# Kernel tuning notes

Hardware: AMD Instinct MI355X
Metric: run time of the kernel (lower is better)

Reference implementation:

```python
import jax, jax.numpy as jnp
import numpy as np

N_NODES = 50000
N_EDGES = 600000
D_IN = 128
D_OUT = 128


def setup_inputs() -> dict:
    key = jax.random.key(0)
    ks = jax.random.split(key, 6)
    gain = float(np.sqrt(2.0))  # relu gain for xavier init
    lim = gain * np.sqrt(6.0 / (D_IN + D_IN))
    pool_w = jax.random.uniform(ks[0], (D_IN, D_IN), jnp.float32, -lim, lim)
    lim2 = gain * np.sqrt(6.0 / (D_IN + D_OUT))
    lin_w = jax.random.uniform(ks[1], (D_OUT, D_IN), jnp.float32, -lim2, lim2)
    return {
        "node_feats": jax.random.normal(ks[2], (N_NODES, D_IN), jnp.float32),
        "src": jax.random.randint(ks[3], (N_EDGES,), 0, N_NODES, jnp.int32),
        "dst": jax.random.randint(ks[4], (N_EDGES,), 0, N_NODES, jnp.int32),
        "e_weight": jax.random.uniform(ks[5], (N_EDGES,), jnp.float32),
        "pool_w": pool_w,
        "pool_b": jnp.zeros((D_IN,), jnp.float32),
        "lin_w": lin_w,
        "lin_b": jnp.zeros((D_OUT,), jnp.float32),
        "bias": jnp.zeros((D_OUT,), jnp.float32),
    }


def reference(node_feats, src, dst, e_weight, pool_w, pool_b, lin_w, lin_b, bias):
    # maxpool aggregator: h_src = relu(pool(x) + pool_bias)   [N, D_IN]
    h_src = jax.nn.relu(node_feats @ pool_w.T + pool_b)
    # u_mul_e message: gather src features, scale by edge weight  [E, D_IN]
    m = h_src[src] * e_weight[:, None]
    # fn.max reduce per destination node; empty mailboxes -> 0
    h_new = jax.ops.segment_max(m, dst, num_segments=N_NODES)
    h_new = jnp.where(jnp.isfinite(h_new), h_new, 0.0)
    # final linear (+its bias) + extra bias parameter
    return h_new @ lin_w.T + lin_b + bias
```

## Files before the change

kernel.cpp:

```cpp
#include <hip/hip_runtime.h>
#include <hip/hip_bf16.h>

#define NN 50000
#define NE 600000
#define DD 128
#define CAP 48

typedef __attribute__((ext_vector_type(8))) short short8_t;
typedef __attribute__((ext_vector_type(4))) short short4_t;
typedef __attribute__((ext_vector_type(4))) float f32x4;

__device__ __forceinline__ short f2bf(float f) {
    union { float f; unsigned u; } v; v.f = f;
    unsigned r = (v.u + 0x7FFFu + ((v.u >> 16) & 1u)) >> 16;
    return (short)r;
}
__device__ __forceinline__ float bflo(unsigned x) { return __uint_as_float(x << 16); }
__device__ __forceinline__ float bfhi(unsigned x) { return __uint_as_float(x & 0xffff0000u); }

__device__ __forceinline__ void gl16(const void* g, void* l) {
    __builtin_amdgcn_global_load_lds(
        (const __attribute__((address_space(1))) unsigned*)g,
        (__attribute__((address_space(3))) unsigned*)l, 16, 0, 0);
}

__global__ __launch_bounds__(512) void gemm1(const float* __restrict__ A,
        const float* __restrict__ Wp, const float* __restrict__ b1,
        unsigned short* __restrict__ hout, const float* __restrict__ Wl,
        unsigned short* __restrict__ wimg, int* __restrict__ counts)
{
    __shared__ short aL[128 * 128];
    __shared__ short wL[128 * 128];
    const int tid = threadIdx.x;
    const int m0 = blockIdx.x * 128;

    {
        int gid = blockIdx.x * 512 + tid;
        if (gid < NN) counts[gid] = 0;
    }
    if (blockIdx.x == 0) {
        #pragma unroll
        for (int i = 0; i < 8; ++i) {
            int idx = (i * 512 + tid) * 4;
            int row = idx >> 7;
            int kk = (idx & 127) ^ ((row & 7) << 3);
            float4 v = *(const float4*)(Wl + row * 128 + kk);
            short4_t s4 = { f2bf(v.x), f2bf(v.y), f2bf(v.z), f2bf(v.w) };
            *(short4_t*)(wimg + idx) = s4;
        }
    }

    #pragma unroll
    for (int i = 0; i < 8; ++i) {
        int flat = i * 2048 + tid * 4;
        int row = flat >> 7, k = flat & 127;
        int gr = m0 + row;
        float4 v = make_float4(0.f, 0.f, 0.f, 0.f);
        if (gr < NN) v = *(const float4*)(A + (size_t)gr * 128 + k);
        short4_t s4 = { f2bf(v.x), f2bf(v.y), f2bf(v.z), f2bf(v.w) };
        *(short4_t*)(aL + ((row * 128 + k) ^ ((row & 7) << 3))) = s4;
    }
    #pragma unroll
    for (int i = 0; i < 8; ++i) {
        int flat = i * 2048 + tid * 4;
        int row = flat >> 7, k = flat & 127;
        float4 v = *(const float4*)(Wp + flat);
        short4_t s4 = { f2bf(v.x), f2bf(v.y), f2bf(v.z), f2bf(v.w) };
        *(short4_t*)(wL + ((row * 128 + k) ^ ((row & 7) << 3))) = s4;
    }
    __syncthreads();

    const int lane = tid & 63, wid = tid >> 6;
    const int l15 = lane & 15, lhi = lane >> 4;
    const int r0 = wid * 16;
    f32x4 acc[8];
    #pragma unroll
    for (int t = 0; t < 8; ++t) acc[t] = f32x4{0.f, 0.f, 0.f, 0.f};

    #pragma unroll
    for (int kk = 0; kk < 4; ++kk) {
        const int k0 = kk * 32 + lhi * 8;
        const int ar = r0 + l15;
        short8_t a = *(short8_t*)(aL + ((ar * 128 + k0) ^ ((ar & 7) << 3)));
        #pragma unroll
        for (int t = 0; t < 8; ++t) {
            const int br = t * 16 + l15;
            short8_t b = *(short8_t*)(wL + ((br * 128 + k0) ^ ((br & 7) << 3)));
            acc[t] = __builtin_amdgcn_mfma_f32_16x16x32_bf16(a, b, acc[t], 0, 0, 0);
        }
    }

    #pragma unroll
    for (int t = 0; t < 8; ++t) {
        const int c = t * 16 + l15;
        float add = b1[c];
        #pragma unroll
        for (int i = 0; i < 4; ++i) {
            int r = m0 + r0 + lhi * 4 + i;
            if (r < NN) {
                float v = fmaxf(acc[t][i] + add, 0.f);
                hout[(size_t)r * 128 + (c ^ ((r & 7) << 3))] = (unsigned short)f2bf(v);
            }
        }
    }
}

__global__ __launch_bounds__(256) void bucket(const int* __restrict__ src,
        const int* __restrict__ dst, const float* __restrict__ ew,
        int* __restrict__ counts, unsigned* __restrict__ edges)
{
    int e = blockIdx.x * 256 + threadIdx.x;
    if (e >= NE) return;
    int d = dst[e];
    int pos = atomicAdd(&counts[d], 1);
    if (pos < CAP)
        edges[(size_t)d * CAP + pos] =
            ((unsigned)src[e] << 16) | (unsigned short)f2bf(ew[e]);
}

template<int NIT>
__device__ __forceinline__ void gat(const unsigned short* __restrict__ hb,
        unsigned p, int deg, int g, int l16, float* m)
{
    #pragma unroll
    for (int it = 0; it < NIT; ++it) {
        const int ia = it * 8 + g, ib = it * 8 + 4 + g;
        unsigned pa = __shfl(p, ia), pb = __shfl(p, ib);
        float wa = (ia < deg) ? __uint_as_float(pa << 16) : 0.f;
        float wb = (ib < deg) ? __uint_as_float(pb << 16) : 0.f;
        unsigned sa = pa >> 16, sb = pb >> 16;
        uint4 ra = *(const uint4*)(hb + (size_t)sa * 128 + ((l16 * 8) ^ ((sa & 7) << 3)));
        uint4 rb = *(const uint4*)(hb + (size_t)sb * 128 + ((l16 * 8) ^ ((sb & 7) << 3)));
        m[0] = fmaxf(m[0], bflo(ra.x) * wa); m[1] = fmaxf(m[1], bfhi(ra.x) * wa);
        m[2] = fmaxf(m[2], bflo(ra.y) * wa); m[3] = fmaxf(m[3], bfhi(ra.y) * wa);
        m[4] = fmaxf(m[4], bflo(ra.z) * wa); m[5] = fmaxf(m[5], bfhi(ra.z) * wa);
        m[6] = fmaxf(m[6], bflo(ra.w) * wa); m[7] = fmaxf(m[7], bfhi(ra.w) * wa);
        m[0] = fmaxf(m[0], bflo(rb.x) * wb); m[1] = fmaxf(m[1], bfhi(rb.x) * wb);
        m[2] = fmaxf(m[2], bflo(rb.y) * wb); m[3] = fmaxf(m[3], bfhi(rb.y) * wb);
        m[4] = fmaxf(m[4], bflo(rb.z) * wb); m[5] = fmaxf(m[5], bfhi(rb.z) * wb);
        m[6] = fmaxf(m[6], bflo(rb.w) * wb); m[7] = fmaxf(m[7], bfhi(rb.w) * wb);
    }
}

__global__ __launch_bounds__(256) void node_max(const unsigned short* __restrict__ hb,
        const int* __restrict__ counts, const unsigned* __restrict__ edges,
        unsigned short* __restrict__ hnew)
{
    int node = blockIdx.x * 4 + (threadIdx.x >> 6);
    if (node >= NN) return;
    const int lane = threadIdx.x & 63;
    const int g = lane >> 4, l16 = lane & 15;
    const int deg = min(counts[node], CAP);
    const unsigned* ep = edges + (size_t)node * CAP;
    unsigned p = (lane < deg) ? ep[lane] : 0u;

    float m[8];
    #pragma unroll
    for (int i = 0; i < 8; ++i) m[i] = 0.f;

    if (deg <= 16)      gat<2>(hb, p, deg, g, l16, m);
    else if (deg <= 32) gat<4>(hb, p, deg, g, l16, m);
    else                gat<6>(hb, p, deg, g, l16, m);

    #pragma unroll
    for (int i = 0; i < 8; ++i) {
        m[i] = fmaxf(m[i], __shfl_xor(m[i], 16));
        m[i] = fmaxf(m[i], __shfl_xor(m[i], 32));
    }

    if (g == 0) {
        uint4 o;
        o.x = ((unsigned)(unsigned short)f2bf(m[1]) << 16) | (unsigned short)f2bf(m[0]);
        o.y = ((unsigned)(unsigned short)f2bf(m[3]) << 16) | (unsigned short)f2bf(m[2]);
        o.z = ((unsigned)(unsigned short)f2bf(m[5]) << 16) | (unsigned short)f2bf(m[4]);
        o.w = ((unsigned)(unsigned short)f2bf(m[7]) << 16) | (unsigned short)f2bf(m[6]);
        *(uint4*)(hnew + (size_t)node * 128 + ((l16 * 8) ^ ((node & 7) << 3))) = o;
    }
}

__global__ __launch_bounds__(512) void gemm2(const unsigned short* __restrict__ Aimg,
        const unsigned short* __restrict__ wimg, const float* __restrict__ b1,
        const float* __restrict__ b2, float* __restrict__ out)
{
    __shared__ short aL[128 * 128];
    __shared__ short wL[128 * 128];
    const int tid = threadIdx.x;
    const int lane = tid & 63, wid = tid >> 6;
    const int m0 = blockIdx.x * 128;

    #pragma unroll
    for (int i = 0; i < 4; ++i) {
        const int soff = i * 4096 + wid * 512;
        gl16(Aimg + (size_t)m0 * 128 + soff + lane * 8, aL + soff);
        gl16(wimg + soff + lane * 8, wL + soff);
    }
    __syncthreads();

    const int l15 = lane & 15, lhi = lane >> 4;
    const int r0 = wid * 16;
    f32x4 acc[8];
    #pragma unroll
    for (int t = 0; t < 8; ++t) acc[t] = f32x4{0.f, 0.f, 0.f, 0.f};

    #pragma unroll
    for (int kk = 0; kk < 4; ++kk) {
        const int k0 = kk * 32 + lhi * 8;
        const int ar = r0 + l15;
        short8_t a = *(short8_t*)(aL + ((ar * 128 + k0) ^ ((ar & 7) << 3)));
        #pragma unroll
        for (int t = 0; t < 8; ++t) {
            const int br = t * 16 + l15;
            short8_t b = *(short8_t*)(wL + ((br * 128 + k0) ^ ((br & 7) << 3)));
            acc[t] = __builtin_amdgcn_mfma_f32_16x16x32_bf16(a, b, acc[t], 0, 0, 0);
        }
    }

    #pragma unroll
    for (int t = 0; t < 8; ++t) {
        const int c = t * 16 + l15;
        float add = b1[c] + b2[c];
        #pragma unroll
        for (int i = 0; i < 4; ++i) {
            int r = m0 + r0 + lhi * 4 + i;
            if (r < NN) out[(size_t)r * 128 + c] = acc[t][i] + add;
        }
    }
}

extern "C" void kernel_launch(void* const* d_in, const int* in_sizes, int n_in,
                              void* d_out, int out_size, void* d_ws, size_t ws_size,
                              hipStream_t stream) {
    const float* node_feats = (const float*)d_in[0];
    const int*   src        = (const int*)d_in[1];
    const int*   dst        = (const int*)d_in[2];
    const float* ew         = (const float*)d_in[3];
    const float* pool_w     = (const float*)d_in[4];
    const float* pool_b     = (const float*)d_in[5];
    const float* lin_w      = (const float*)d_in[6];
    const float* lin_b      = (const float*)d_in[7];
    const float* bias       = (const float*)d_in[8];
    float* out = (float*)d_out;

    char* w0 = (char*)d_ws;
    unsigned short* hsrc = (unsigned short*)w0;  w0 += (size_t)NN * DD * 2;
    unsigned short* hnew = (unsigned short*)w0;  w0 += (size_t)NN * DD * 2;
    int* counts = (int*)w0;                      w0 += (size_t)NN * 4;
    unsigned* edges = (unsigned*)w0;             w0 += (size_t)NN * CAP * 4;
    unsigned short* wimg = (unsigned short*)w0;  w0 += (size_t)DD * DD * 2;

    const int gemm_grid = (NN + 127) / 128;
    gemm1<<<gemm_grid, 512, 0, stream>>>(node_feats, pool_w, pool_b, hsrc,
                                         lin_w, wimg, counts);

    bucket<<<(NE + 255) / 256, 256, 0, stream>>>(src, dst, ew, counts, edges);

    node_max<<<(NN + 3) / 4, 256, 0, stream>>>(hsrc, counts, edges, hnew);

    gemm2<<<gemm_grid, 512, 0, stream>>>(hnew, wimg, lin_b, bias, out);
}
```

Before: 164.8 us.

## Pre-convert weights once, read B fragments from global, halve GEMM row tiles

A new prep kernel converts pool_w and lin_w to bf16 once. Previously every gemm1 block converted the full fp32 pool_w into LDS. Both GEMMs now use 64-row tiles with 8 waves split into 4 row groups by 2 column halves. A fragments stay in registers and B fragments are loaded directly from global/L2 instead of LDS. The h_src swizzle is dropped so node_max gathers unswizzled rows; this adds one kernel launch and relies on cache hits for the weight reads.

```diff
diff --git a/kernel.cpp b/kernel.cpp
--- a/kernel.cpp
+++ b/kernel.cpp
@@ -24,34 +24,34 @@
         (__attribute__((address_space(3))) unsigned*)l, 16, 0, 0);
 }
 
+__global__ __launch_bounds__(256) void prep(const float* __restrict__ pw,
+        const float* __restrict__ lw, unsigned short* __restrict__ w1,
+        unsigned short* __restrict__ w2)
+{
+    const int b = blockIdx.x, t = threadIdx.x;
+    const float* s = (b < 16) ? pw : lw;
+    unsigned short* d = (b < 16) ? w1 : w2;
+    int base = (b & 15) * 1024 + t * 4;
+    float4 v = *(const float4*)(s + base);
+    short4_t s4 = { f2bf(v.x), f2bf(v.y), f2bf(v.z), f2bf(v.w) };
+    *(short4_t*)(d + base) = s4;
+}
+
 __global__ __launch_bounds__(512) void gemm1(const float* __restrict__ A,
-        const float* __restrict__ Wp, const float* __restrict__ b1,
-        unsigned short* __restrict__ hout, const float* __restrict__ Wl,
-        unsigned short* __restrict__ wimg, int* __restrict__ counts)
-{
-    __shared__ short aL[128 * 128];
-    __shared__ short wL[128 * 128];
+        const unsigned short* __restrict__ Wb, const float* __restrict__ b1,
+        unsigned short* __restrict__ hout, int* __restrict__ counts)
+{
+    __shared__ short aL[64 * 128];
     const int tid = threadIdx.x;
-    const int m0 = blockIdx.x * 128;
+    const int m0 = blockIdx.x * 64;
 
     {
         int gid = blockIdx.x * 512 + tid;
         if (gid < NN) counts[gid] = 0;
     }
-    if (blockIdx.x == 0) {
-        #pragma unroll
-        for (int i = 0; i < 8; ++i) {
-            int idx = (i * 512 + tid) * 4;
-            int row = idx >> 7;
-            int kk = (idx & 127) ^ ((row & 7) << 3);
-            float4 v = *(const float4*)(Wl + row * 128 + kk);
-            short4_t s4 = { f2bf(v.x), f2bf(v.y), f2bf(v.z), f2bf(v.w) };
-            *(short4_t*)(wimg + idx) = s4;
-        }
-    }
-
-    #pragma unroll
-    for (int i = 0; i < 8; ++i) {
+
+    #pragma unroll
+    for (int i = 0; i < 4; ++i) {
         int flat = i * 2048 + tid * 4;
         int row = flat >> 7, k = flat & 127;
         int gr = m0 + row;
@@ -60,46 +60,44 @@
         short4_t s4 = { f2bf(v.x), f2bf(v.y), f2bf(v.z), f2bf(v.w) };
         *(short4_t*)(aL + ((row * 128 + k) ^ ((row & 7) << 3))) = s4;
     }
-    #pragma unroll
-    for (int i = 0; i < 8; ++i) {
-        int flat = i * 2048 + tid * 4;
-        int row = flat >> 7, k = flat & 127;
-        float4 v = *(const float4*)(Wp + flat);
-        short4_t s4 = { f2bf(v.x), f2bf(v.y), f2bf(v.z), f2bf(v.w) };
-        *(short4_t*)(wL + ((row * 128 + k) ^ ((row & 7) << 3))) = s4;
-    }
     __syncthreads();
 
     const int lane = tid & 63, wid = tid >> 6;
     const int l15 = lane & 15, lhi = lane >> 4;
-    const int r0 = wid * 16;
-    f32x4 acc[8];
-    #pragma unroll
-    for (int t = 0; t < 8; ++t) acc[t] = f32x4{0.f, 0.f, 0.f, 0.f};
-
+    const int rg = wid & 3, cs = wid >> 2;
+    const int r0 = rg * 16;
+
+    short8_t af[4];
     #pragma unroll
     for (int kk = 0; kk < 4; ++kk) {
-        const int k0 = kk * 32 + lhi * 8;
         const int ar = r0 + l15;
-        short8_t a = *(short8_t*)(aL + ((ar * 128 + k0) ^ ((ar & 7) << 3)));
-        #pragma unroll
-        for (int t = 0; t < 8; ++t) {
-            const int br = t * 16 + l15;
-            short8_t b = *(short8_t*)(wL + ((br * 128 + k0) ^ ((br & 7) << 3)));
-            acc[t] = __builtin_amdgcn_mfma_f32_16x16x32_bf16(a, b, acc[t], 0, 0, 0);
-        }
-    }
-
-    #pragma unroll
-    for (int t = 0; t < 8; ++t) {
-        const int c = t * 16 + l15;
+        af[kk] = *(short8_t*)(aL + ((ar * 128 + kk * 32 + lhi * 8) ^ ((ar & 7) << 3)));
+    }
+
+    f32x4 acc[4];
+    #pragma unroll
+    for (int t = 0; t < 4; ++t) acc[t] = f32x4{0.f, 0.f, 0.f, 0.f};
+
+    #pragma unroll
+    for (int t = 0; t < 4; ++t) {
+        const int br = cs * 64 + t * 16 + l15;
+        #pragma unroll
+        for (int kk = 0; kk < 4; ++kk) {
+            short8_t b = *(const short8_t*)(Wb + br * 128 + kk * 32 + lhi * 8);
+            acc[t] = __builtin_amdgcn_mfma_f32_16x16x32_bf16(af[kk], b, acc[t], 0, 0, 0);
+        }
+    }
+
+    #pragma unroll
+    for (int t = 0; t < 4; ++t) {
+        const int c = cs * 64 + t * 16 + l15;
         float add = b1[c];
         #pragma unroll
         for (int i = 0; i < 4; ++i) {
             int r = m0 + r0 + lhi * 4 + i;
             if (r < NN) {
                 float v = fmaxf(acc[t][i] + add, 0.f);
-                hout[(size_t)r * 128 + (c ^ ((r & 7) << 3))] = (unsigned short)f2bf(v);
+                hout[(size_t)r * 128 + c] = (unsigned short)f2bf(v);
             }
         }
     }
@@ -128,9 +126,8 @@
         unsigned pa = __shfl(p, ia), pb = __shfl(p, ib);
         float wa = (ia < deg) ? __uint_as_float(pa << 16) : 0.f;
         float wb = (ib < deg) ? __uint_as_float(pb << 16) : 0.f;
-        unsigned sa = pa >> 16, sb = pb >> 16;
-        uint4 ra = *(const uint4*)(hb + (size_t)sa * 128 + ((l16 * 8) ^ ((sa & 7) << 3)));
-        uint4 rb = *(const uint4*)(hb + (size_t)sb * 128 + ((l16 * 8) ^ ((sb & 7) << 3)));
+        uint4 ra = *(const uint4*)(hb + (size_t)(pa >> 16) * 128 + l16 * 8);
+        uint4 rb = *(const uint4*)(hb + (size_t)(pb >> 16) * 128 + l16 * 8);
         m[0] = fmaxf(m[0], bflo(ra.x) * wa); m[1] = fmaxf(m[1], bfhi(ra.x) * wa);
         m[2] = fmaxf(m[2], bflo(ra.y) * wa); m[3] = fmaxf(m[3], bfhi(ra.y) * wa);
         m[4] = fmaxf(m[4], bflo(ra.z) * wa); m[5] = fmaxf(m[5], bfhi(ra.z) * wa);
@@ -179,45 +176,49 @@
 }
 
 __global__ __launch_bounds__(512) void gemm2(const unsigned short* __restrict__ Aimg,
-        const unsigned short* __restrict__ wimg, const float* __restrict__ b1,
+        const unsigned short* __restrict__ Wb, const float* __restrict__ b1,
         const float* __restrict__ b2, float* __restrict__ out)
 {
-    __shared__ short aL[128 * 128];
-    __shared__ short wL[128 * 128];
+    __shared__ short aL[64 * 128];
     const int tid = threadIdx.x;
     const int lane = tid & 63, wid = tid >> 6;
-    const int m0 = blockIdx.x * 128;
-
-    #pragma unroll
-    for (int i = 0; i < 4; ++i) {
-        const int soff = i * 4096 + wid * 512;
+    const int m0 = blockIdx.x * 64;
+
+    #pragma unroll
+    for (int i = 0; i < 2; ++i) {
+        const int soff = wid * 1024 + i * 512;
         gl16(Aimg + (size_t)m0 * 128 + soff + lane * 8, aL + soff);
-        gl16(wimg + soff + lane * 8, wL + soff);
     }
     __syncthreads();
 
     const int l15 = lane & 15, lhi = lane >> 4;
-    const int r0 = wid * 16;
-    f32x4 acc[8];
-    #pragma unroll
-    for (int t = 0; t < 8; ++t) acc[t] = f32x4{0.f, 0.f, 0.f, 0.f};
-
+    const int rg = wid & 3, cs = wid >> 2;
+    const int r0 = rg * 16;
+
+    short8_t af[4];
     #pragma unroll
     for (int kk = 0; kk < 4; ++kk) {
-        const int k0 = kk * 32 + lhi * 8;
         const int ar = r0 + l15;
-        short8_t a = *(short8_t*)(aL + ((ar * 128 + k0) ^ ((ar & 7) << 3)));
-        #pragma unroll
-        for (int t = 0; t < 8; ++t) {
-            const int br = t * 16 + l15;
-            short8_t b = *(short8_t*)(wL + ((br * 128 + k0) ^ ((br & 7) << 3)));
-            acc[t] = __builtin_amdgcn_mfma_f32_16x16x32_bf16(a, b, acc[t], 0, 0, 0);
-        }
-    }
-
-    #pragma unroll
-    for (int t = 0; t < 8; ++t) {
-        const int c = t * 16 + l15;
+        af[kk] = *(short8_t*)(aL + ((ar * 128 + kk * 32 + lhi * 8) ^ ((ar & 7) << 3)));
+    }
+
+    f32x4 acc[4];
+    #pragma unroll
+    for (int t = 0; t < 4; ++t) acc[t] = f32x4{0.f, 0.f, 0.f, 0.f};
+
+    #pragma unroll
+    for (int t = 0; t < 4; ++t) {
+        const int br = cs * 64 + t * 16 + l15;
+        #pragma unroll
+        for (int kk = 0; kk < 4; ++kk) {
+            short8_t b = *(const short8_t*)(Wb + br * 128 + kk * 32 + lhi * 8);
+            acc[t] = __builtin_amdgcn_mfma_f32_16x16x32_bf16(af[kk], b, acc[t], 0, 0, 0);
+        }
+    }
+
+    #pragma unroll
+    for (int t = 0; t < 4; ++t) {
+        const int c = cs * 64 + t * 16 + l15;
         float add = b1[c] + b2[c];
         #pragma unroll
         for (int i = 0; i < 4; ++i) {
@@ -246,15 +247,17 @@
     unsigned short* hnew = (unsigned short*)w0;  w0 += (size_t)NN * DD * 2;
     int* counts = (int*)w0;                      w0 += (size_t)NN * 4;
     unsigned* edges = (unsigned*)w0;             w0 += (size_t)NN * CAP * 4;
-    unsigned short* wimg = (unsigned short*)w0;  w0 += (size_t)DD * DD * 2;
-
-    const int gemm_grid = (NN + 127) / 128;
-    gemm1<<<gemm_grid, 512, 0, stream>>>(node_feats, pool_w, pool_b, hsrc,
-                                         lin_w, wimg, counts);
+    unsigned short* w1b = (unsigned short*)w0;   w0 += (size_t)DD * DD * 2;
+    unsigned short* w2b = (unsigned short*)w0;   w0 += (size_t)DD * DD * 2;
+
+    prep<<<32, 256, 0, stream>>>(pool_w, lin_w, w1b, w2b);
+
+    const int g_grid = (NN + 63) / 64;
+    gemm1<<<g_grid, 512, 0, stream>>>(node_feats, w1b, pool_b, hsrc, counts);
 
     bucket<<<(NE + 255) / 256, 256, 0, stream>>>(src, dst, ew, counts, edges);
 
     node_max<<<(NN + 3) / 4, 256, 0, stream>>>(hsrc, counts, edges, hnew);
 
-    gemm2<<<gemm_grid, 512, 0, stream>>>(hnew, wimg, lin_b, bias, out);
-}
+    gemm2<<<g_grid, 512, 0, stream>>>(hnew, w2b, lin_b, bias, out);
+}
```

Measured after the change: 187.6 us. 13.8% more time.
